# Kernel optimization log

Measured on AMD Instinct MI355X. Metric: run time of the kernel, lower is better.

## Reference

```python
import jax, jax.numpy as jnp
import numpy as np

NUM_CATEGORIES = 32
INPUT_DIM = 1024
HIDDEN_DIM = 2048
B, T = 64, 256


def setup_inputs() -> dict:
    key = jax.random.key(0)
    k_x, k_cat, k_w = jax.random.split(key, 3)
    x = jax.random.normal(k_x, (B, T, INPUT_DIM), dtype=jnp.float32)
    cat_ids = jax.random.randint(k_cat, (B,), 0, NUM_CATEGORIES, dtype=jnp.int32)
    W = 0.02 * jax.random.normal(k_w, (NUM_CATEGORIES, INPUT_DIM, HIDDEN_DIM), dtype=jnp.float32)
    b = jnp.zeros((NUM_CATEGORIES, HIDDEN_DIM), dtype=jnp.float32)
    return {"x": x, "cat_ids": cat_ids, "W": W, "b": b}


def reference(x, cat_ids, W, b):
    # Gather per-sample weight [B, in, hid] and bias [B, hid], then batched matmul.
    selected_W = W[cat_ids]            # [B, INPUT_DIM, HIDDEN_DIM]
    selected_b = b[cat_ids]            # [B, HIDDEN_DIM]
    out = jnp.einsum('bti,bih->bth', x, selected_W) + selected_b[:, None, :]
    return out
```

## Files before the change

### kernel.cpp

```cpp
#include <hip/hip_runtime.h>
#include <hip/hip_bf16.h>

#define NUM_CAT 32
#define IN_DIM 1024
#define HID_DIM 2048
#define T_DIM 256
#define B_DIM 64

typedef __attribute__((ext_vector_type(4))) float floatx4;
typedef __attribute__((ext_vector_type(8))) short shortx8;

__device__ __forceinline__ unsigned pack2(float a, float b) {
  __hip_bfloat162 h2 = __float22bfloat162_rn(make_float2(a, b));
  unsigned u;
  __builtin_memcpy(&u, &h2, 4);
  return u;
}

__device__ __forceinline__ int swz(int row) {
  return ((row & 7) << 4) ^ ((row & 8) << 2);
}

__global__ __launch_bounds__(256) void cat_linear_fused_kernel(
    const float* __restrict__ x, const int* __restrict__ cat_ids,
    const float* __restrict__ W, const float* __restrict__ bias,
    float* __restrict__ out) {
  const int nt = blockIdx.x;
  const int mt = blockIdx.y;
  const int b  = blockIdx.z;
  const int tid = threadIdx.x;
  const int c = cat_ids[b];

  __shared__ __attribute__((aligned(16))) unsigned short As[128 * 64];
  __shared__ __attribute__((aligned(16))) unsigned short Bs[128 * 64];

  const int lane = tid & 63;
  const int wv   = tid >> 6;
  const int wm   = (wv >> 1) * 64;
  const int wn   = (wv & 1) * 64;
  const int l16  = lane & 15;
  const int quad = lane >> 4;

  const int ar = tid >> 3;
  const int au = tid & 7;
  const int bn4 = (tid & 31) * 4;
  const int bk8 = (tid >> 5) * 8;

  const float* xb = x + ((size_t)b * T_DIM + (size_t)mt * 128) * IN_DIM;
  const float* Wc = W + (size_t)c * IN_DIM * HID_DIM + (size_t)nt * 128;

  floatx4 acc[4][4] = {};

  for (int ks = 0; ks < IN_DIM / 64; ++ks) {
    const int k0 = ks * 64;

    #pragma unroll
    for (int i = 0; i < 4; ++i) {
      const int m = i * 32 + ar;
      const float* ap = xb + (size_t)m * IN_DIM + k0 + au * 8;
      const float4 v0 = *reinterpret_cast<const float4*>(ap);
      const float4 v1 = *reinterpret_cast<const float4*>(ap + 4);
      union { shortx8 s8; unsigned u[4]; } pk;
      pk.u[0] = pack2(v0.x, v0.y);
      pk.u[1] = pack2(v0.z, v0.w);
      pk.u[2] = pack2(v1.x, v1.y);
      pk.u[3] = pack2(v1.z, v1.w);
      *reinterpret_cast<shortx8*>(
          (char*)As + m * 128 + ((au * 16) ^ swz(m))) = pk.s8;
    }

    {
      const float* wp = Wc + (size_t)(k0 + bk8) * HID_DIM + bn4;
      const float4 w0 = *reinterpret_cast<const float4*>(wp + 0 * HID_DIM);
      const float4 w1 = *reinterpret_cast<const float4*>(wp + 1 * HID_DIM);
      const float4 w2 = *reinterpret_cast<const float4*>(wp + 2 * HID_DIM);
      const float4 w3 = *reinterpret_cast<const float4*>(wp + 3 * HID_DIM);
      const float4 w4 = *reinterpret_cast<const float4*>(wp + 4 * HID_DIM);
      const float4 w5 = *reinterpret_cast<const float4*>(wp + 5 * HID_DIM);
      const float4 w6 = *reinterpret_cast<const float4*>(wp + 6 * HID_DIM);
      const float4 w7 = *reinterpret_cast<const float4*>(wp + 7 * HID_DIM);
      union { shortx8 s8; unsigned u[4]; } pk;
      pk.u[0] = pack2(w0.x, w1.x); pk.u[1] = pack2(w2.x, w3.x);
      pk.u[2] = pack2(w4.x, w5.x); pk.u[3] = pack2(w6.x, w7.x);
      *reinterpret_cast<shortx8*>(
          (char*)Bs + (bn4 + 0) * 128 + ((bk8 * 2) ^ swz(bn4 + 0))) = pk.s8;
      pk.u[0] = pack2(w0.y, w1.y); pk.u[1] = pack2(w2.y, w3.y);
      pk.u[2] = pack2(w4.y, w5.y); pk.u[3] = pack2(w6.y, w7.y);
      *reinterpret_cast<shortx8*>(
          (char*)Bs + (bn4 + 1) * 128 + ((bk8 * 2) ^ swz(bn4 + 1))) = pk.s8;
      pk.u[0] = pack2(w0.z, w1.z); pk.u[1] = pack2(w2.z, w3.z);
      pk.u[2] = pack2(w4.z, w5.z); pk.u[3] = pack2(w6.z, w7.z);
      *reinterpret_cast<shortx8*>(
          (char*)Bs + (bn4 + 2) * 128 + ((bk8 * 2) ^ swz(bn4 + 2))) = pk.s8;
      pk.u[0] = pack2(w0.w, w1.w); pk.u[1] = pack2(w2.w, w3.w);
      pk.u[2] = pack2(w4.w, w5.w); pk.u[3] = pack2(w6.w, w7.w);
      *reinterpret_cast<shortx8*>(
          (char*)Bs + (bn4 + 3) * 128 + ((bk8 * 2) ^ swz(bn4 + 3))) = pk.s8;
    }

    __syncthreads();

    #pragma unroll
    for (int s = 0; s < 2; ++s) {
      shortx8 af[4], bfr[4];
      #pragma unroll
      for (int i = 0; i < 4; ++i) {
        const int row = wm + i * 16 + l16;
        af[i] = *reinterpret_cast<const shortx8*>(
            (const char*)As + row * 128 + ((s * 64 + quad * 16) ^ swz(row)));
      }
      #pragma unroll
      for (int j = 0; j < 4; ++j) {
        const int row = wn + j * 16 + l16;
        bfr[j] = *reinterpret_cast<const shortx8*>(
            (const char*)Bs + row * 128 + ((s * 64 + quad * 16) ^ swz(row)));
      }
      #pragma unroll
      for (int i = 0; i < 4; ++i)
        #pragma unroll
        for (int j = 0; j < 4; ++j)
          acc[i][j] = __builtin_amdgcn_mfma_f32_16x16x32_bf16(af[i], bfr[j], acc[i][j], 0, 0, 0);
    }

    __syncthreads();
  }

  float* outp = out + ((size_t)b * T_DIM + (size_t)mt * 128) * HID_DIM + nt * 128;
  const float* bp = bias + (size_t)c * HID_DIM + nt * 128;
  #pragma unroll
  for (int j = 0; j < 4; ++j) {
    const float bj = bp[wn + j * 16 + l16];
    #pragma unroll
    for (int i = 0; i < 4; ++i) {
      #pragma unroll
      for (int r = 0; r < 4; ++r) {
        const int m = wm + i * 16 + quad * 4 + r;
        outp[(size_t)m * HID_DIM + wn + j * 16 + l16] = acc[i][j][r] + bj;
      }
    }
  }
}

extern "C" void kernel_launch(void* const* d_in, const int* in_sizes, int n_in,
                              void* d_out, int out_size, void* d_ws, size_t ws_size,
                              hipStream_t stream) {
  const float* x    = (const float*)d_in[0];
  const int*   cat  = (const int*)d_in[1];
  const float* W    = (const float*)d_in[2];
  const float* bias = (const float*)d_in[3];
  float* out = (float*)d_out;

  dim3 grid(HID_DIM / 128, T_DIM / 128, B_DIM);
  hipLaunchKernelGGL(cat_linear_fused_kernel, grid, dim3(256), 0, stream,
                     x, cat, W, bias, out);
}
```

Measured before the change: 547.0 us.

## Double-buffer LDS with register prefetch and sort batches by category for W reuse

```diff
diff --git a/kernel.cpp b/kernel.cpp
--- a/kernel.cpp
+++ b/kernel.cpp
@@ -27,12 +27,25 @@
     float* __restrict__ out) {
   const int nt = blockIdx.x;
   const int mt = blockIdx.y;
-  const int b  = blockIdx.z;
   const int tid = threadIdx.x;
+
+  __shared__ int bsel;
+  {
+    const int i = tid & 63;
+    const int ci = cat_ids[i];
+    int pos = 0;
+    for (int j = 0; j < 64; ++j) {
+      const int cj = cat_ids[j];
+      pos += (cj < ci || (cj == ci && j < i)) ? 1 : 0;
+    }
+    if (tid < 64 && pos == (int)blockIdx.z) bsel = i;
+  }
+  __syncthreads();
+  const int b = bsel;
   const int c = cat_ids[b];
 
-  __shared__ __attribute__((aligned(16))) unsigned short As[128 * 64];
-  __shared__ __attribute__((aligned(16))) unsigned short Bs[128 * 64];
+  __shared__ __attribute__((aligned(16))) unsigned short As[2][128 * 64];
+  __shared__ __attribute__((aligned(16))) unsigned short Bs[2][128 * 64];
 
   const int lane = tid & 63;
   const int wv   = tid >> 6;
@@ -51,51 +64,66 @@
 
   floatx4 acc[4][4] = {};
 
+  float4 pa[8];
+  float4 pw[8];
+
+  auto issueA = [&](int ks) {
+    const int k0 = ks * 64;
+    #pragma unroll
+    for (int i = 0; i < 4; ++i) {
+      const float* ap = xb + (size_t)(i * 32 + ar) * IN_DIM + k0 + au * 8;
+      pa[2 * i]     = *reinterpret_cast<const float4*>(ap);
+      pa[2 * i + 1] = *reinterpret_cast<const float4*>(ap + 4);
+    }
+  };
+  auto issueW = [&](int ks) {
+    const float* wp = Wc + (size_t)(ks * 64 + bk8) * HID_DIM + bn4;
+    #pragma unroll
+    for (int r = 0; r < 8; ++r)
+      pw[r] = *reinterpret_cast<const float4*>(wp + (size_t)r * HID_DIM);
+  };
+
+  issueA(0);
+  issueW(0);
+
   for (int ks = 0; ks < IN_DIM / 64; ++ks) {
-    const int k0 = ks * 64;
+    unsigned short* Asb = As[ks & 1];
+    unsigned short* Bsb = Bs[ks & 1];
 
     #pragma unroll
     for (int i = 0; i < 4; ++i) {
       const int m = i * 32 + ar;
-      const float* ap = xb + (size_t)m * IN_DIM + k0 + au * 8;
-      const float4 v0 = *reinterpret_cast<const float4*>(ap);
-      const float4 v1 = *reinterpret_cast<const float4*>(ap + 4);
       union { shortx8 s8; unsigned u[4]; } pk;
-      pk.u[0] = pack2(v0.x, v0.y);
-      pk.u[1] = pack2(v0.z, v0.w);
-      pk.u[2] = pack2(v1.x, v1.y);
-      pk.u[3] = pack2(v1.z, v1.w);
+      pk.u[0] = pack2(pa[2 * i].x, pa[2 * i].y);
+      pk.u[1] = pack2(pa[2 * i].z, pa[2 * i].w);
+      pk.u[2] = pack2(pa[2 * i + 1].x, pa[2 * i + 1].y);
+      pk.u[3] = pack2(pa[2 * i + 1].z, pa[2 * i + 1].w);
       *reinterpret_cast<shortx8*>(
-          (char*)As + m * 128 + ((au * 16) ^ swz(m))) = pk.s8;
+          (char*)Asb + m * 128 + ((au * 16) ^ swz(m))) = pk.s8;
+    }
+    {
+      union { shortx8 s8; unsigned u[4]; } pk;
+      pk.u[0] = pack2(pw[0].x, pw[1].x); pk.u[1] = pack2(pw[2].x, pw[3].x);
+      pk.u[2] = pack2(pw[4].x, pw[5].x); pk.u[3] = pack2(pw[6].x, pw[7].x);
+      *reinterpret_cast<shortx8*>(
+          (char*)Bsb + (bn4 + 0) * 128 + ((bk8 * 2) ^ swz(bn4 + 0))) = pk.s8;
+      pk.u[0] = pack2(pw[0].y, pw[1].y); pk.u[1] = pack2(pw[2].y, pw[3].y);
+      pk.u[2] = pack2(pw[4].y, pw[5].y); pk.u[3] = pack2(pw[6].y, pw[7].y);
+      *reinterpret_cast<shortx8*>(
+          (char*)Bsb + (bn4 + 1) * 128 + ((bk8 * 2) ^ swz(bn4 + 1))) = pk.s8;
+      pk.u[0] = pack2(pw[0].z, pw[1].z); pk.u[1] = pack2(pw[2].z, pw[3].z);
+      pk.u[2] = pack2(pw[4].z, pw[5].z); pk.u[3] = pack2(pw[6].z, pw[7].z);
+      *reinterpret_cast<shortx8*>(
+          (char*)Bsb + (bn4 + 2) * 128 + ((bk8 * 2) ^ swz(bn4 + 2))) = pk.s8;
+      pk.u[0] = pack2(pw[0].w, pw[1].w); pk.u[1] = pack2(pw[2].w, pw[3].w);
+      pk.u[2] = pack2(pw[4].w, pw[5].w); pk.u[3] = pack2(pw[6].w, pw[7].w);
+      *reinterpret_cast<shortx8*>(
+          (char*)Bsb + (bn4 + 3) * 128 + ((bk8 * 2) ^ swz(bn4 + 3))) = pk.s8;
     }
 
-    {
-      const float* wp = Wc + (size_t)(k0 + bk8) * HID_DIM + bn4;
-      const float4 w0 = *reinterpret_cast<const float4*>(wp + 0 * HID_DIM);
-      const float4 w1 = *reinterpret_cast<const float4*>(wp + 1 * HID_DIM);
-      const float4 w2 = *reinterpret_cast<const float4*>(wp + 2 * HID_DIM);
-      const float4 w3 = *reinterpret_cast<const float4*>(wp + 3 * HID_DIM);
-      const float4 w4 = *reinterpret_cast<const float4*>(wp + 4 * HID_DIM);
-      const float4 w5 = *reinterpret_cast<const float4*>(wp + 5 * HID_DIM);
-      const float4 w6 = *reinterpret_cast<const float4*>(wp + 6 * HID_DIM);
-      const float4 w7 = *reinterpret_cast<const float4*>(wp + 7 * HID_DIM);
-      union { shortx8 s8; unsigned u[4]; } pk;
-      pk.u[0] = pack2(w0.x, w1.x); pk.u[1] = pack2(w2.x, w3.x);
-      pk.u[2] = pack2(w4.x, w5.x); pk.u[3] = pack2(w6.x, w7.x);
-      *reinterpret_cast<shortx8*>(
-          (char*)Bs + (bn4 + 0) * 128 + ((bk8 * 2) ^ swz(bn4 + 0))) = pk.s8;
-      pk.u[0] = pack2(w0.y, w1.y); pk.u[1] = pack2(w2.y, w3.y);
-      pk.u[2] = pack2(w4.y, w5.y); pk.u[3] = pack2(w6.y, w7.y);
-      *reinterpret_cast<shortx8*>(
-          (char*)Bs + (bn4 + 1) * 128 + ((bk8 * 2) ^ swz(bn4 + 1))) = pk.s8;
-      pk.u[0] = pack2(w0.z, w1.z); pk.u[1] = pack2(w2.z, w3.z);
-      pk.u[2] = pack2(w4.z, w5.z); pk.u[3] = pack2(w6.z, w7.z);
-      *reinterpret_cast<shortx8*>(
-          (char*)Bs + (bn4 + 2) * 128 + ((bk8 * 2) ^ swz(bn4 + 2))) = pk.s8;
-      pk.u[0] = pack2(w0.w, w1.w); pk.u[1] = pack2(w2.w, w3.w);
-      pk.u[2] = pack2(w4.w, w5.w); pk.u[3] = pack2(w6.w, w7.w);
-      *reinterpret_cast<shortx8*>(
-          (char*)Bs + (bn4 + 3) * 128 + ((bk8 * 2) ^ swz(bn4 + 3))) = pk.s8;
+    if (ks < IN_DIM / 64 - 1) {
+      issueA(ks + 1);
+      issueW(ks + 1);
     }
 
     __syncthreads();
@@ -107,13 +135,13 @@
       for (int i = 0; i < 4; ++i) {
         const int row = wm + i * 16 + l16;
         af[i] = *reinterpret_cast<const shortx8*>(
-            (const char*)As + row * 128 + ((s * 64 + quad * 16) ^ swz(row)));
+            (const char*)Asb + row * 128 + ((s * 64 + quad * 16) ^ swz(row)));
       }
       #pragma unroll
       for (int j = 0; j < 4; ++j) {
         const int row = wn + j * 16 + l16;
         bfr[j] = *reinterpret_cast<const shortx8*>(
-            (const char*)Bs + row * 128 + ((s * 64 + quad * 16) ^ swz(row)));
+            (const char*)Bsb + row * 128 + ((s * 64 + quad * 16) ^ swz(row)));
       }
       #pragma unroll
       for (int i = 0; i < 4; ++i)
@@ -121,8 +149,6 @@
         for (int j = 0; j < 4; ++j)
           acc[i][j] = __builtin_amdgcn_mfma_f32_16x16x32_bf16(af[i], bfr[j], acc[i][j], 0, 0, 0);
     }
-
-    __syncthreads();
   }
 
   float* outp = out + ((size_t)b * T_DIM + (size_t)mt * 128) * HID_DIM + nt * 128;
```

Measured after the change: 503.3 us. 1.09x faster.
